# Optimization experiments

Hardware: AMD Instinct MI355X
Metric: run time of the kernel (lower is better)

Reference implementation:

```python
import jax, jax.numpy as jnp
import numpy as np

H = 8
LN_EPS = 1e-5


def setup_inputs() -> dict:
    key = jax.random.key(0)
    ks = jax.random.split(key, 4)
    B, S, D = 4, 2048, 1024
    x = jax.random.normal(ks[0], (B, S, D), dtype=jnp.float32)
    sc = 1.0 / np.sqrt(D)
    Wq = jax.random.normal(ks[1], (D, D), dtype=jnp.float32) * sc
    Wk = jax.random.normal(ks[2], (D, D), dtype=jnp.float32) * sc
    Wv = jax.random.normal(ks[3], (D, D * H), dtype=jnp.float32) * sc
    return {
        "x": x,
        "Wq": Wq, "bq": jnp.zeros((D,), jnp.float32),
        "Wk": Wk, "bk": jnp.zeros((D,), jnp.float32),
        "Wv": Wv, "bv": jnp.zeros((D * H,), jnp.float32),
        "gamma": jnp.ones((D,), jnp.float32),
        "beta": jnp.zeros((D,), jnp.float32),
    }


def reference(x, Wq, bq, Wk, bk, Wv, bv, gamma, beta):
    B, S, D = x.shape
    dk = D // H
    # LayerNorm (applied first, as in the torch module)
    mu = jnp.mean(x, axis=-1, keepdims=True)
    var = jnp.mean(jnp.square(x - mu), axis=-1, keepdims=True)
    xn = (x - mu) * jax.lax.rsqrt(var + LN_EPS) * gamma + beta
    # projections
    q = (xn @ Wq + bq).reshape(B, S, H, dk).transpose(0, 2, 1, 3)      # [B,H,S,dk]
    k = (xn @ Wk + bk).reshape(B, S, H, dk).transpose(0, 2, 1, 3)      # [B,H,S,dk]
    v = (xn @ Wv + bv).reshape(B, S, H, D).transpose(0, 2, 1, 3)       # [B,H,S,D] wide values
    scores = jnp.einsum("bhsd,bhtd->bhst", q, k) / jnp.sqrt(jnp.asarray(dk, x.dtype))
    p = jax.nn.softmax(scores, axis=-1)                                 # [B,H,S,S]
    att = jnp.einsum("bhst,bhtd->bhsd", p, v)                           # [B,H,S,D]
    # faithful replication of torch's raw .view(-1,B,D,H) + head-sum + .view(B,-1,D)
    out = att.reshape(S, B, D, H).sum(axis=-1).reshape(B, S, D)
    return out
```

## Files before the change

### kernel.cpp

```cpp
#include <hip/hip_runtime.h>
#include <hip/hip_bf16.h>


typedef __bf16 bf16_t;
typedef __bf16 bf16x8 __attribute__((ext_vector_type(8)));
typedef __bf16 bf16x4 __attribute__((ext_vector_type(4)));
typedef float  f32x4  __attribute__((ext_vector_type(4)));

#define AS1 __attribute__((address_space(1)))
#define AS3 __attribute__((address_space(3)))

static __device__ __forceinline__ void gload_lds16(const void* g, void* l) {
  __builtin_amdgcn_global_load_lds((const AS1 void*)g, (AS3 void*)l, 16, 0, 0);
}

__global__ __launch_bounds__(256) void k_wvsum(const float* __restrict__ Wv,
                                               float* __restrict__ tmp) {
  const int k = blockIdx.x;
  const float* row = Wv + (size_t)k * 8192;
  float* orow = tmp + (size_t)k * 1024;
  #pragma unroll
  for (int p = 0; p < 4; ++p) {
    const int n = p * 256 + threadIdx.x;
    const int base = ((n >> 7) << 10) + ((n & 127) << 3);
    const float4 a = *(const float4*)(row + base);
    const float4 b = *(const float4*)(row + base + 4);
    orow[n] = a.x + a.y + a.z + a.w + b.x + b.y + b.z + b.w;
  }
}

__global__ __launch_bounds__(256) void k_transpose(const float* __restrict__ src,
                                                   bf16_t* __restrict__ dst) {
  __shared__ float tile[32][33];
  const int tx = threadIdx.x, ty = threadIdx.y;
  const int c0 = blockIdx.x * 32, r0 = blockIdx.y * 32;
  #pragma unroll
  for (int j = 0; j < 4; ++j)
    tile[ty + j * 8][tx] = src[(size_t)(r0 + ty + j * 8) * 1024 + c0 + tx];
  __syncthreads();
  #pragma unroll
  for (int j = 0; j < 4; ++j)
    dst[(size_t)(c0 + ty + j * 8) * 1024 + r0 + tx] = (bf16_t)tile[tx][ty + j * 8];
}

__global__ __launch_bounds__(256) void k_bias(const float* __restrict__ bq,
                                              const float* __restrict__ bk,
                                              const float* __restrict__ bv,
                                              float* __restrict__ bias) {
  const int i = blockIdx.x * 256 + threadIdx.x;
  float v;
  if (i < 1024) v = bq[i];
  else if (i < 2048) v = bk[i - 1024];
  else {
    const int n = i - 2048;
    const int base = ((n >> 7) << 10) + ((n & 127) << 3);
    v = 0.f;
    #pragma unroll
    for (int j = 0; j < 8; ++j) v += bv[base + j];
  }
  bias[i] = v;
}

__global__ __launch_bounds__(256) void k_ln(const float* __restrict__ x,
                                            const float* __restrict__ gamma,
                                            const float* __restrict__ beta,
                                            bf16_t* __restrict__ xn) {
  const int row = blockIdx.x, tid = threadIdx.x;
  const float4 v = ((const float4*)x)[(size_t)row * 256 + tid];
  float s  = v.x + v.y + v.z + v.w;
  float ss = v.x * v.x + v.y * v.y + v.z * v.z + v.w * v.w;
  #pragma unroll
  for (int off = 32; off >= 1; off >>= 1) {
    s  += __shfl_down(s, off);
    ss += __shfl_down(ss, off);
  }
  __shared__ float red[8];
  if ((tid & 63) == 0) { red[tid >> 6] = s; red[4 + (tid >> 6)] = ss; }
  __syncthreads();
  s  = red[0] + red[1] + red[2] + red[3];
  ss = red[4] + red[5] + red[6] + red[7];
  const float mu   = s * (1.0f / 1024.0f);
  const float rstd = rsqrtf(ss * (1.0f / 1024.0f) - mu * mu + 1e-5f);
  const float4 g = ((const float4*)gamma)[tid];
  const float4 b = ((const float4*)beta)[tid];
  bf16x4 o;
  o[0] = (bf16_t)((v.x - mu) * rstd * g.x + b.x);
  o[1] = (bf16_t)((v.y - mu) * rstd * g.y + b.y);
  o[2] = (bf16_t)((v.z - mu) * rstd * g.z + b.z);
  o[3] = (bf16_t)((v.w - mu) * rstd * g.w + b.w);
  *(bf16x4*)(xn + (size_t)row * 1024 + tid * 4) = o;
}

__global__ __launch_bounds__(256) void k_gemm(const bf16_t* __restrict__ Ag,
                                              const bf16_t* __restrict__ Bg,
                                              const float* __restrict__ bias,
                                              bf16_t* __restrict__ Cg) {
  __shared__ __align__(16) bf16_t As[128 * 64];
  __shared__ __align__(16) bf16_t Bs[128 * 64];
  const int tid = threadIdx.x, w = tid >> 6, l = tid & 63;
  const int m0 = blockIdx.y * 128, n0 = blockIdx.x * 128;
  const int wm = (w >> 1) * 64, wn = (w & 1) * 64;
  const int qr = l & 15, ko = (l >> 4) * 8;
  const int srow   = l >> 3;
  const int schunk = 8 * ((l & 7) ^ srow);

  f32x4 acc[4][4];
  #pragma unroll
  for (int i = 0; i < 4; ++i)
    #pragma unroll
    for (int j = 0; j < 4; ++j) acc[i][j] = (f32x4){0.f, 0.f, 0.f, 0.f};

  for (int kt = 0; kt < 1024; kt += 64) {
    #pragma unroll
    for (int c = 0; c < 4; ++c) {
      const int cc = w * 4 + c;
      const int row = cc * 8 + srow;
      gload_lds16(Ag + (size_t)(m0 + row) * 1024 + kt + schunk, As + cc * 512);
      gload_lds16(Bg + (size_t)(n0 + row) * 1024 + kt + schunk, Bs + cc * 512);
    }
    __syncthreads();
    #pragma unroll
    for (int kk = 0; kk < 2; ++kk) {
      const int eo = (kk * 32 + ko) ^ ((qr & 7) << 3);
      bf16x8 afr[4], bfr[4];
      #pragma unroll
      for (int x = 0; x < 4; ++x) {
        afr[x] = *(const bf16x8*)(As + (wm + x * 16 + qr) * 64 + eo);
        bfr[x] = *(const bf16x8*)(Bs + (wn + x * 16 + qr) * 64 + eo);
      }
      #pragma unroll
      for (int mi = 0; mi < 4; ++mi)
        #pragma unroll
        for (int ni = 0; ni < 4; ++ni)
          acc[mi][ni] = __builtin_amdgcn_mfma_f32_16x16x32_bf16(
              afr[mi], bfr[ni], acc[mi][ni], 0, 0, 0);
    }
    __syncthreads();
  }
  #pragma unroll
  for (int ni = 0; ni < 4; ++ni) {
    const int col = n0 + wn + ni * 16 + qr;
    const float bc = bias[col];
    #pragma unroll
    for (int mi = 0; mi < 4; ++mi)
      #pragma unroll
      for (int r = 0; r < 4; ++r) {
        const int row = m0 + wm + mi * 16 + (l >> 4) * 4 + r;
        Cg[(size_t)row * 3072 + col] = (bf16_t)(acc[mi][ni][r] + bc);
      }
  }
}

__global__ __launch_bounds__(256) void k_attn(const bf16_t* __restrict__ QKV,
                                              float* __restrict__ out) {
  __shared__ __align__(16) bf16_t Kt[64 * 128];
  __shared__ __align__(16) bf16_t Vt[128 * 64];
  __shared__ __align__(16) bf16_t Pl[4][32 * 64];

  const int tid = threadIdx.x, w = tid >> 6, l = tid & 63;
  const int b = blockIdx.y >> 3, h = blockIdx.y & 7;
  const int q0 = blockIdx.x * 128 + w * 32;
  const int qr = l & 15, ko = (l >> 4) * 8;

  const bf16_t* Qb = QKV + (size_t)b * 2048 * 3072 + h * 128;
  const bf16_t* Kb = Qb + 1024;
  const bf16_t* Vb = Qb + 2048;

  bf16x8 aq[2][4];
  #pragma unroll
  for (int mi = 0; mi < 2; ++mi)
    #pragma unroll
    for (int kk = 0; kk < 4; ++kk)
      aq[mi][kk] = *(const bf16x8*)(Qb + (size_t)(q0 + mi * 16 + qr) * 3072 + kk * 32 + ko);

  f32x4 o[2][8];
  float mrun[2][4], lrun[2][4];
  #pragma unroll
  for (int mi = 0; mi < 2; ++mi) {
    #pragma unroll
    for (int ni = 0; ni < 8; ++ni) o[mi][ni] = (f32x4){0.f, 0.f, 0.f, 0.f};
    #pragma unroll
    for (int r = 0; r < 4; ++r) { mrun[mi][r] = -1e30f; lrun[mi][r] = 0.f; }
  }

  const int krow_in = l >> 4;
  const int kchunk  = l & 15;
  const int vt_loc  = w * 16 + qr;

  for (int t0 = 0; t0 < 2048; t0 += 64) {
    #pragma unroll
    for (int c = 0; c < 4; ++c) {
      const int cc = w * 4 + c;
      const int row = cc * 4 + krow_in;
      const int selem = 8 * (kchunk ^ (row & 7));
      gload_lds16(Kb + (size_t)(t0 + row) * 3072 + selem, Kt + cc * 512);
    }
    #pragma unroll
    for (int p = 0; p < 4; ++p) {
      const int chunk = (l >> 4) * 4 + p;
      const bf16x8 v8 = *(const bf16x8*)(Vb + (size_t)(t0 + vt_loc) * 3072 + chunk * 8);
      #pragma unroll
      for (int j = 0; j < 8; ++j) {
        const int dg = chunk * 8 + j;
        Vt[dg * 64 + (vt_loc ^ (j << 3))] = v8[j];
      }
    }
    __syncthreads();

    f32x4 s[2][4];
    #pragma unroll
    for (int mi = 0; mi < 2; ++mi)
      #pragma unroll
      for (int ni = 0; ni < 4; ++ni) s[mi][ni] = (f32x4){0.f, 0.f, 0.f, 0.f};
    #pragma unroll
    for (int kk = 0; kk < 4; ++kk) {
      const int eo = (kk * 32 + ko) ^ ((qr & 7) << 3);
      #pragma unroll
      for (int ni = 0; ni < 4; ++ni) {
        const bf16x8 bfr = *(const bf16x8*)(Kt + (ni * 16 + qr) * 128 + eo);
        s[0][ni] = __builtin_amdgcn_mfma_f32_16x16x32_bf16(aq[0][kk], bfr, s[0][ni], 0, 0, 0);
        s[1][ni] = __builtin_amdgcn_mfma_f32_16x16x32_bf16(aq[1][kk], bfr, s[1][ni], 0, 0, 0);
      }
    }

    const float sc = 0.08838834764831845f;
    #pragma unroll
    for (int mi = 0; mi < 2; ++mi)
      #pragma unroll
      for (int r = 0; r < 4; ++r) {
        const float z0 = s[mi][0][r] * sc, z1 = s[mi][1][r] * sc;
        const float z2 = s[mi][2][r] * sc, z3 = s[mi][3][r] * sc;
        float mx = fmaxf(fmaxf(z0, z1), fmaxf(z2, z3));
        #pragma unroll
        for (int off = 1; off < 16; off <<= 1) mx = fmaxf(mx, __shfl_xor(mx, off));
        const float mold = mrun[mi][r];
        const float mnew = fmaxf(mold, mx);
        const float fac  = __expf(mold - mnew);
        const float p0 = __expf(z0 - mnew), p1 = __expf(z1 - mnew);
        const float p2 = __expf(z2 - mnew), p3 = __expf(z3 - mnew);
        float ps = p0 + p1 + p2 + p3;
        #pragma unroll
        for (int off = 1; off < 16; off <<= 1) ps += __shfl_xor(ps, off);
        lrun[mi][r] = lrun[mi][r] * fac + ps;
        mrun[mi][r] = mnew;
        #pragma unroll
        for (int ni = 0; ni < 8; ++ni) o[mi][ni][r] *= fac;
        const int prow = mi * 16 + (l >> 4) * 4 + r;
        const int px = (prow & 7) << 3;
        bf16_t* pr = &Pl[w][prow * 64];
        pr[(0 * 16 + qr) ^ px] = (bf16_t)p0;
        pr[(1 * 16 + qr) ^ px] = (bf16_t)p1;
        pr[(2 * 16 + qr) ^ px] = (bf16_t)p2;
        pr[(3 * 16 + qr) ^ px] = (bf16_t)p3;
      }

    #pragma unroll
    for (int kk = 0; kk < 2; ++kk) {
      const int eo = (kk * 32 + ko) ^ ((qr & 7) << 3);
      const bf16x8 ap0 = *(const bf16x8*)(&Pl[w][(0 * 16 + qr) * 64 + eo]);
      const bf16x8 ap1 = *(const bf16x8*)(&Pl[w][(16 + qr) * 64 + eo]);
      #pragma unroll
      for (int ni = 0; ni < 8; ++ni) {
        const bf16x8 bv = *(const bf16x8*)(Vt + (ni * 16 + qr) * 64 + eo);
        o[0][ni] = __builtin_amdgcn_mfma_f32_16x16x32_bf16(ap0, bv, o[0][ni], 0, 0, 0);
        o[1][ni] = __builtin_amdgcn_mfma_f32_16x16x32_bf16(ap1, bv, o[1][ni], 0, 0, 0);
      }
    }
    __syncthreads();
  }

  #pragma unroll
  for (int mi = 0; mi < 2; ++mi)
    #pragma unroll
    for (int r = 0; r < 4; ++r) {
      const int qrow = q0 + mi * 16 + (l >> 4) * 4 + r;
      const float inv = 1.0f / lrun[mi][r];
      float* orow = out + ((size_t)b * 2048 + h * 256 + (qrow >> 3)) * 1024
                  + (qrow & 7) * 128;
      #pragma unroll
      for (int ni = 0; ni < 8; ++ni)
        orow[ni * 16 + qr] = o[mi][ni][r] * inv;
    }
}

extern "C" void kernel_launch(void* const* d_in, const int* in_sizes, int n_in,
                              void* d_out, int out_size, void* d_ws, size_t ws_size,
                              hipStream_t stream) {
  const float* x     = (const float*)d_in[0];
  const float* Wq    = (const float*)d_in[1];
  const float* bq    = (const float*)d_in[2];
  const float* Wk    = (const float*)d_in[3];
  const float* bk    = (const float*)d_in[4];
  const float* Wv    = (const float*)d_in[5];
  const float* bv    = (const float*)d_in[6];
  const float* gamma = (const float*)d_in[7];
  const float* beta  = (const float*)d_in[8];
  float* out = (float*)d_out;

  char* ws = (char*)d_ws;
  size_t off = 0;
  bf16_t* WT  = (bf16_t*)(ws + off); off += (size_t)3072 * 1024 * 2;
  float*  bias = (float*)(ws + off); off += (size_t)3072 * 4;
  off = (off + 255) & ~(size_t)255;
  bf16_t* xn  = (bf16_t*)(ws + off); off += (size_t)8192 * 1024 * 2;
  bf16_t* QKV = (bf16_t*)(ws + off); off += (size_t)8192 * 3072 * 2;
  float*  tmp = (float*)(ws + off);  off += (size_t)1024 * 1024 * 4;

  const dim3 tb(32, 8), tg(32, 32);
  k_wvsum<<<1024, 256, 0, stream>>>(Wv, tmp);
  k_transpose<<<tg, tb, 0, stream>>>(Wq, WT);
  k_transpose<<<tg, tb, 0, stream>>>(Wk, WT + (size_t)1024 * 1024);
  k_transpose<<<tg, tb, 0, stream>>>(tmp, WT + (size_t)2048 * 1024);
  k_bias<<<12, 256, 0, stream>>>(bq, bk, bv, bias);
  k_ln<<<8192, 256, 0, stream>>>(x, gamma, beta, xn);
  k_gemm<<<dim3(24, 64), 256, 0, stream>>>(xn, WT, bias, QKV);
  k_attn<<<dim3(16, 32), 256, 0, stream>>>(QKV, out);
}
```

Baseline: 413.9 us.

## Pipeline attention K/V loads, keep P in registers, lazy rescale, staged output

Rewrites the flash-attention kernel. K is triple-buffered via global-to-LDS loads and V is double-buffered through registers, so the next tile's loads overlap the current tile's compute with only one barrier per iteration. S is computed transposed so P stays in registers and feeds 16x16x16 MFMAs directly, which removes the per-warp P round trip through LDS. The softmax max is reduced with two shuffles per row, and the O rescale is skipped unless the max grows by more than a threshold. The block index is remapped, and output goes through LDS so global writes are coalesced float4 stores. The cost is more LDS and register pressure, plus extra code complexity around the deferred rescale.

```diff
diff --git a/kernel.cpp b/kernel.cpp
--- a/kernel.cpp
+++ b/kernel.cpp
@@ -5,7 +5,10 @@
 typedef __bf16 bf16_t;
 typedef __bf16 bf16x8 __attribute__((ext_vector_type(8)));
 typedef __bf16 bf16x4 __attribute__((ext_vector_type(4)));
+typedef short  s16x4  __attribute__((ext_vector_type(4)));
 typedef float  f32x4  __attribute__((ext_vector_type(4)));
+typedef unsigned short u16;
+typedef unsigned int   u32;
 
 #define AS1 __attribute__((address_space(1)))
 #define AS3 __attribute__((address_space(3)))
@@ -13,6 +16,12 @@
 static __device__ __forceinline__ void gload_lds16(const void* g, void* l) {
   __builtin_amdgcn_global_load_lds((const AS1 void*)g, (AS3 void*)l, 16, 0, 0);
 }
+
+static __device__ __forceinline__ float vmax4(f32x4 v) {
+  return fmaxf(fmaxf(v[0], v[1]), fmaxf(v[2], v[3]));
+}
+
+#define MFMA16(a, b, c) __builtin_amdgcn_mfma_f32_16x16x16bf16_1k(a, b, c, 0, 0, 0)
 
 __global__ __launch_bounds__(256) void k_wvsum(const float* __restrict__ Wv,
                                                float* __restrict__ tmp) {
@@ -151,16 +160,21 @@
   }
 }
 
-__global__ __launch_bounds__(256) void k_attn(const bf16_t* __restrict__ QKV,
-                                              float* __restrict__ out) {
-  __shared__ __align__(16) bf16_t Kt[64 * 128];
-  __shared__ __align__(16) bf16_t Vt[128 * 64];
-  __shared__ __align__(16) bf16_t Pl[4][32 * 64];
+__global__ __launch_bounds__(256, 2) void k_attn(const bf16_t* __restrict__ QKV,
+                                                 float* __restrict__ out) {
+  __shared__ __align__(16) union {
+    struct { bf16_t K[3][64 * 128]; bf16_t VT[2][128 * 64]; } st;
+    float Os[4][16 * 132];
+  } sm;
 
   const int tid = threadIdx.x, w = tid >> 6, l = tid & 63;
-  const int b = blockIdx.y >> 3, h = blockIdx.y & 7;
-  const int q0 = blockIdx.x * 128 + w * 32;
-  const int qr = l & 15, ko = (l >> 4) * 8;
+  const int g = l >> 4, qr = l & 15;
+  const int bid = blockIdx.x;
+  const int slot = bid >> 3;
+  const int bh = (bid & 7) * 4 + (slot >> 4);
+  const int qt = slot & 15;
+  const int b = bh >> 3, h = bh & 7;
+  const int q0 = qt * 128 + w * 32;
 
   const bf16_t* Qb = QKV + (size_t)b * 2048 * 3072 + h * 128;
   const bf16_t* Kb = Qb + 1024;
@@ -171,116 +185,174 @@
   for (int mi = 0; mi < 2; ++mi)
     #pragma unroll
     for (int kk = 0; kk < 4; ++kk)
-      aq[mi][kk] = *(const bf16x8*)(Qb + (size_t)(q0 + mi * 16 + qr) * 3072 + kk * 32 + ko);
+      aq[mi][kk] = *(const bf16x8*)(Qb + (size_t)(q0 + mi * 16 + qr) * 3072 + kk * 32 + g * 8);
 
   f32x4 o[2][8];
-  float mrun[2][4], lrun[2][4];
+  #pragma unroll
+  for (int mi = 0; mi < 2; ++mi)
+    #pragma unroll
+    for (int d = 0; d < 8; ++d) o[mi][d] = (f32x4){0.f, 0.f, 0.f, 0.f};
+  float m0 = -1e30f, m1 = -1e30f, l0 = 0.f, l1 = 0.f;
+
+  const int vt = w * 16 + (l >> 2);
+  const int vc = (l & 3) * 8;
+  const int tp2 = (w * 8 + (l >> 3)) * 2;
+  const int par = (l >> 2) & 1;
+
+  union U8 { bf16x8 v; u16 u[8]; u32 d[4]; };
+
+  #pragma unroll
+  for (int c = 0; c < 4; ++c) {
+    const int cc = w * 4 + c;
+    const int krow = cc * 4 + g;
+    gload_lds16(Kb + (size_t)krow * 3072 + 8 * ((l & 15) ^ (krow & 7)),
+                sm.st.K[0] + cc * 512);
+  }
+  bf16x8 vreg[4], vnext[4];
+  #pragma unroll
+  for (int p = 0; p < 4; ++p)
+    vreg[p] = *(const bf16x8*)(Vb + (size_t)vt * 3072 + vc + p * 32);
+
+  const float sc = 0.08838834764831845f;
+  int kc = 0, vbuf = 0;
+
+  for (int it = 0; it < 32; ++it) {
+    const int t0 = it * 64;
+    {
+      bf16_t* VTw = sm.st.VT[vbuf];
+      #pragma unroll
+      for (int p = 0; p < 4; ++p) {
+        U8 mine, part;
+        mine.v = vreg[p];
+        #pragma unroll
+        for (int q2 = 0; q2 < 4; ++q2) part.d[q2] = __shfl_xor(mine.d[q2], 4);
+        #pragma unroll
+        for (int jj = 0; jj < 4; ++jj) {
+          const int j = par * 4 + jj;
+          const int dv = vc + p * 32 + j;
+          const u32 val = par ? ((u32)part.u[j] | ((u32)mine.u[j] << 16))
+                              : ((u32)mine.u[j] | ((u32)part.u[j] << 16));
+          *(u32*)(VTw + dv * 64 + (tp2 ^ (8 * (dv & 7)))) = val;
+        }
+      }
+    }
+    const int kn = (kc == 2) ? 0 : kc + 1;
+    if (it < 31) {
+      const int tn = t0 + 64;
+      #pragma unroll
+      for (int c = 0; c < 4; ++c) {
+        const int cc = w * 4 + c;
+        const int krow = cc * 4 + g;
+        gload_lds16(Kb + (size_t)(tn + krow) * 3072 + 8 * ((l & 15) ^ (krow & 7)),
+                    sm.st.K[kn] + cc * 512);
+      }
+      #pragma unroll
+      for (int p = 0; p < 4; ++p)
+        vnext[p] = *(const bf16x8*)(Vb + (size_t)(tn + vt) * 3072 + vc + p * 32);
+    }
+    if (it < 31) asm volatile("s_waitcnt vmcnt(8) lgkmcnt(0)" ::: "memory");
+    else         asm volatile("s_waitcnt vmcnt(0) lgkmcnt(0)" ::: "memory");
+    __builtin_amdgcn_s_barrier();
+    __builtin_amdgcn_sched_barrier(0);
+
+    const bf16_t* Kc = sm.st.K[kc];
+    f32x4 s[2][4];
+    #pragma unroll
+    for (int mi = 0; mi < 2; ++mi)
+      #pragma unroll
+      for (int ni = 0; ni < 4; ++ni) s[mi][ni] = (f32x4){0.f, 0.f, 0.f, 0.f};
+    __builtin_amdgcn_s_setprio(1);
+    #pragma unroll
+    for (int kk = 0; kk < 4; ++kk) {
+      const int eo = (kk * 32 + g * 8) ^ ((qr & 7) << 3);
+      #pragma unroll
+      for (int ni = 0; ni < 4; ++ni) {
+        const bf16x8 ka = *(const bf16x8*)(Kc + (ni * 16 + qr) * 128 + eo);
+        s[0][ni] = __builtin_amdgcn_mfma_f32_16x16x32_bf16(ka, aq[0][kk], s[0][ni], 0, 0, 0);
+        s[1][ni] = __builtin_amdgcn_mfma_f32_16x16x32_bf16(ka, aq[1][kk], s[1][ni], 0, 0, 0);
+      }
+    }
+    __builtin_amdgcn_s_setprio(0);
+
+    float mx0 = fmaxf(fmaxf(vmax4(s[0][0]), vmax4(s[0][1])),
+                      fmaxf(vmax4(s[0][2]), vmax4(s[0][3])));
+    float mx1 = fmaxf(fmaxf(vmax4(s[1][0]), vmax4(s[1][1])),
+                      fmaxf(vmax4(s[1][2]), vmax4(s[1][3])));
+    mx0 = fmaxf(mx0, __shfl_xor(mx0, 16)); mx0 = fmaxf(mx0, __shfl_xor(mx0, 32));
+    mx1 = fmaxf(mx1, __shfl_xor(mx1, 16)); mx1 = fmaxf(mx1, __shfl_xor(mx1, 32));
+    const float zx0 = mx0 * sc, zx1 = mx1 * sc;
+    if (!__all(fmaxf(zx0 - m0, zx1 - m1) <= 8.0f)) {
+      const float n0 = fmaxf(m0, zx0), n1 = fmaxf(m1, zx1);
+      const float f0 = __expf(m0 - n0), f1 = __expf(m1 - n1);
+      l0 *= f0; l1 *= f1; m0 = n0; m1 = n1;
+      #pragma unroll
+      for (int d = 0; d < 8; ++d) {
+        #pragma unroll
+        for (int r = 0; r < 4; ++r) { o[0][d][r] *= f0; o[1][d][r] *= f1; }
+      }
+    }
+    s16x4 pf[2][4];
+    float ps0 = 0.f, ps1 = 0.f;
+    #pragma unroll
+    for (int ni = 0; ni < 4; ++ni) {
+      bf16x4 t0v, t1v;
+      #pragma unroll
+      for (int r = 0; r < 4; ++r) {
+        const float p0 = __expf(fmaf(s[0][ni][r], sc, -m0));
+        const float p1 = __expf(fmaf(s[1][ni][r], sc, -m1));
+        ps0 += p0; ps1 += p1;
+        t0v[r] = (bf16_t)p0; t1v[r] = (bf16_t)p1;
+      }
+      pf[0][ni] = __builtin_bit_cast(s16x4, t0v);
+      pf[1][ni] = __builtin_bit_cast(s16x4, t1v);
+    }
+    ps0 += __shfl_xor(ps0, 16); ps0 += __shfl_xor(ps0, 32);
+    ps1 += __shfl_xor(ps1, 16); ps1 += __shfl_xor(ps1, 32);
+    l0 += ps0; l1 += ps1;
+
+    const bf16_t* VTc = sm.st.VT[vbuf];
+    #pragma unroll
+    for (int ni = 0; ni < 4; ++ni) {
+      __builtin_amdgcn_s_setprio(1);
+      #pragma unroll
+      for (int dvt = 0; dvt < 8; ++dvt) {
+        const int dvA = dvt * 16 + qr;
+        const s16x4 vf = __builtin_bit_cast(s16x4,
+            *(const bf16x4*)(VTc + dvA * 64 + ((ni * 16 + g * 4) ^ (8 * (dvA & 7)))));
+        o[0][dvt] = MFMA16(vf, pf[0][ni], o[0][dvt]);
+        o[1][dvt] = MFMA16(vf, pf[1][ni], o[1][dvt]);
+      }
+      __builtin_amdgcn_s_setprio(0);
+    }
+
+    #pragma unroll
+    for (int p = 0; p < 4; ++p) vreg[p] = vnext[p];
+    kc = kn; vbuf ^= 1;
+  }
+
+  const float inv0 = 1.0f / l0, inv1 = 1.0f / l1;
+  float* Osw = sm.Os[w];
+  const size_t obase = ((size_t)b * 2048 + (size_t)h * 256) * 1024;
   #pragma unroll
   for (int mi = 0; mi < 2; ++mi) {
-    #pragma unroll
-    for (int ni = 0; ni < 8; ++ni) o[mi][ni] = (f32x4){0.f, 0.f, 0.f, 0.f};
-    #pragma unroll
-    for (int r = 0; r < 4; ++r) { mrun[mi][r] = -1e30f; lrun[mi][r] = 0.f; }
-  }
-
-  const int krow_in = l >> 4;
-  const int kchunk  = l & 15;
-  const int vt_loc  = w * 16 + qr;
-
-  for (int t0 = 0; t0 < 2048; t0 += 64) {
-    #pragma unroll
-    for (int c = 0; c < 4; ++c) {
-      const int cc = w * 4 + c;
-      const int row = cc * 4 + krow_in;
-      const int selem = 8 * (kchunk ^ (row & 7));
-      gload_lds16(Kb + (size_t)(t0 + row) * 3072 + selem, Kt + cc * 512);
-    }
-    #pragma unroll
-    for (int p = 0; p < 4; ++p) {
-      const int chunk = (l >> 4) * 4 + p;
-      const bf16x8 v8 = *(const bf16x8*)(Vb + (size_t)(t0 + vt_loc) * 3072 + chunk * 8);
-      #pragma unroll
-      for (int j = 0; j < 8; ++j) {
-        const int dg = chunk * 8 + j;
-        Vt[dg * 64 + (vt_loc ^ (j << 3))] = v8[j];
-      }
-    }
     __syncthreads();
-
-    f32x4 s[2][4];
-    #pragma unroll
-    for (int mi = 0; mi < 2; ++mi)
-      #pragma unroll
-      for (int ni = 0; ni < 4; ++ni) s[mi][ni] = (f32x4){0.f, 0.f, 0.f, 0.f};
-    #pragma unroll
-    for (int kk = 0; kk < 4; ++kk) {
-      const int eo = (kk * 32 + ko) ^ ((qr & 7) << 3);
-      #pragma unroll
-      for (int ni = 0; ni < 4; ++ni) {
-        const bf16x8 bfr = *(const bf16x8*)(Kt + (ni * 16 + qr) * 128 + eo);
-        s[0][ni] = __builtin_amdgcn_mfma_f32_16x16x32_bf16(aq[0][kk], bfr, s[0][ni], 0, 0, 0);
-        s[1][ni] = __builtin_amdgcn_mfma_f32_16x16x32_bf16(aq[1][kk], bfr, s[1][ni], 0, 0, 0);
-      }
-    }
-
-    const float sc = 0.08838834764831845f;
-    #pragma unroll
-    for (int mi = 0; mi < 2; ++mi)
+    const float inv = mi ? inv1 : inv0;
+    #pragma unroll
+    for (int dvt = 0; dvt < 8; ++dvt)
       #pragma unroll
       for (int r = 0; r < 4; ++r) {
-        const float z0 = s[mi][0][r] * sc, z1 = s[mi][1][r] * sc;
-        const float z2 = s[mi][2][r] * sc, z3 = s[mi][3][r] * sc;
-        float mx = fmaxf(fmaxf(z0, z1), fmaxf(z2, z3));
-        #pragma unroll
-        for (int off = 1; off < 16; off <<= 1) mx = fmaxf(mx, __shfl_xor(mx, off));
-        const float mold = mrun[mi][r];
-        const float mnew = fmaxf(mold, mx);
-        const float fac  = __expf(mold - mnew);
-        const float p0 = __expf(z0 - mnew), p1 = __expf(z1 - mnew);
-        const float p2 = __expf(z2 - mnew), p3 = __expf(z3 - mnew);
-        float ps = p0 + p1 + p2 + p3;
-        #pragma unroll
-        for (int off = 1; off < 16; off <<= 1) ps += __shfl_xor(ps, off);
-        lrun[mi][r] = lrun[mi][r] * fac + ps;
-        mrun[mi][r] = mnew;
-        #pragma unroll
-        for (int ni = 0; ni < 8; ++ni) o[mi][ni][r] *= fac;
-        const int prow = mi * 16 + (l >> 4) * 4 + r;
-        const int px = (prow & 7) << 3;
-        bf16_t* pr = &Pl[w][prow * 64];
-        pr[(0 * 16 + qr) ^ px] = (bf16_t)p0;
-        pr[(1 * 16 + qr) ^ px] = (bf16_t)p1;
-        pr[(2 * 16 + qr) ^ px] = (bf16_t)p2;
-        pr[(3 * 16 + qr) ^ px] = (bf16_t)p3;
-      }
-
-    #pragma unroll
-    for (int kk = 0; kk < 2; ++kk) {
-      const int eo = (kk * 32 + ko) ^ ((qr & 7) << 3);
-      const bf16x8 ap0 = *(const bf16x8*)(&Pl[w][(0 * 16 + qr) * 64 + eo]);
-      const bf16x8 ap1 = *(const bf16x8*)(&Pl[w][(16 + qr) * 64 + eo]);
-      #pragma unroll
-      for (int ni = 0; ni < 8; ++ni) {
-        const bf16x8 bv = *(const bf16x8*)(Vt + (ni * 16 + qr) * 64 + eo);
-        o[0][ni] = __builtin_amdgcn_mfma_f32_16x16x32_bf16(ap0, bv, o[0][ni], 0, 0, 0);
-        o[1][ni] = __builtin_amdgcn_mfma_f32_16x16x32_bf16(ap1, bv, o[1][ni], 0, 0, 0);
-      }
-    }
+        const float val = (mi ? o[1][dvt][r] : o[0][dvt][r]) * inv;
+        Osw[qr * 132 + dvt * 16 + g * 4 + r] = val;
+      }
     __syncthreads();
-  }
-
-  #pragma unroll
-  for (int mi = 0; mi < 2; ++mi)
-    #pragma unroll
-    for (int r = 0; r < 4; ++r) {
-      const int qrow = q0 + mi * 16 + (l >> 4) * 4 + r;
-      const float inv = 1.0f / lrun[mi][r];
-      float* orow = out + ((size_t)b * 2048 + h * 256 + (qrow >> 3)) * 1024
-                  + (qrow & 7) * 128;
-      #pragma unroll
-      for (int ni = 0; ni < 8; ++ni)
-        orow[ni * 16 + qr] = o[mi][ni][r] * inv;
-    }
+    const int row = l >> 2;
+    const int cb  = (l & 3) * 32;
+    const int q = q0 + mi * 16 + row;
+    float* dst = out + obase + (size_t)(q >> 3) * 1024 + (q & 7) * 128 + cb;
+    #pragma unroll
+    for (int e = 0; e < 8; ++e)
+      *(float4*)(dst + e * 4) = *(const float4*)(Osw + row * 132 + cb + e * 4);
+  }
 }
 
 extern "C" void kernel_launch(void* const* d_in, const int* in_sizes, int n_in,
@@ -314,5 +386,5 @@
   k_bias<<<12, 256, 0, stream>>>(bq, bk, bv, bias);
   k_ln<<<8192, 256, 0, stream>>>(x, gamma, beta, xn);
   k_gemm<<<dim3(24, 64), 256, 0, stream>>>(xn, WT, bias, QKV);
-  k_attn<<<dim3(16, 32), 256, 0, stream>>>(QKV, out);
-}
+  k_attn<<<512, 256, 0, stream>>>(QKV, out);
+}
```

Result: faster. 343.1 us (-17.1%).
